# Performance work log

Hardware: AMD Instinct MI355X
Metric: run time of the kernel (lower is better)

Reference implementation:

```python
import jax, jax.numpy as jnp
import numpy as np

C = 1536
MA = 1536
NEG_SLOPE = 0.2


def setup_inputs() -> dict:
    key = jax.random.key(0)
    ks = jax.random.split(key, 11)
    s = 1.0 / np.sqrt(C)

    def u(k, shape):
        return jax.random.uniform(k, shape, jnp.float32, -s, s)

    return {
        "x": jax.random.normal(ks[0], (1, C), jnp.float32),
        "lw0": u(ks[1], (C, C)), "lb0": u(ks[2], (C,)),
        "lw1": u(ks[3], (C, C)), "lb1": u(ks[4], (C,)),
        "lw2": u(ks[5], (1, C)), "lb2": u(ks[6], (1,)),
        "W_ih": u(ks[7], (3, C, C)), "b_ih": u(ks[8], (3, C)),
        "W_hh": u(ks[9], (3, C, C)), "b_hh": u(ks[10], (3, C)),
        "max_atoms": MA,
    }


def reference(x, lw0, lb0, lw1, lb1, lw2, lb2, W_ih, b_ih, W_hh, b_hh, max_atoms):
    c_dim = x.shape[-1]
    x = x.reshape(1, c_dim)

    act = lambda v: jax.nn.leaky_relu(v, NEG_SLOPE)
    # LinearOutputStack(channels, 3, out_channels=1): 2 hidden layers + output head
    h = act(x @ lw0.T + lb0)
    h = act(h @ lw1.T + lb1)
    l = h @ lw2.T + lb2                       # [1, 1]
    length = jnp.clip(jnp.abs(l), 0.0, 0.9999)
    c = jnp.floor(length[0, 0] * max_atoms).astype(jnp.int32) + 1  # #valid steps

    hid0 = jnp.zeros((3, c_dim), x.dtype).at[0].set(x[0])  # hid[0] = x
    inp0 = jnp.zeros((c_dim,), x.dtype)

    def step(carry, _):
        inp, hid = carry
        cur = inp
        new_hid = []
        for layer in range(3):  # stacked relu-RNN, one timestep
            nh = jax.nn.relu(cur @ W_ih[layer].T + b_ih[layer]
                             + hid[layer] @ W_hh[layer].T + b_hh[layer])
            new_hid.append(nh)
            cur = nh
        return (cur, jnp.stack(new_hid)), cur

    _, seq = jax.lax.scan(step, (inp0, hid0), None, length=max_atoms)  # [MA, C]
    # Original returns only the first c rows; we pad with zeros for static shape.
    mask = (jnp.arange(max_atoms) < c)[:, None]
    seq = jnp.where(mask, seq, jnp.zeros((), seq.dtype))
    return seq, length
```

## Files before the change

kernel.cpp:

```cpp
#include <hip/hip_runtime.h>
#include <math.h>

#define C     1536
#define MA    1536
#define NWG   256
#define TPB   384
#define NEG   0.2f

#define WS_H0    0
#define WS_H1    (C)
#define WS_HB    (2*C)
#define WS_CNUM  (6*C)
#define WS_ARR   (6*C + 64)

#define WSCALE   (32760.0f * 39.191835884530846f)
#define WINV     (1.0f / WSCALE)

#define WL_WORDS (36 * 768)

__global__ void ve_init(unsigned* w) {
    for (int k = threadIdx.x; k < NWG * 16; k += blockDim.x)
        __hip_atomic_store(&w[WS_ARR + k], 0u, __ATOMIC_RELAXED, __HIP_MEMORY_SCOPE_AGENT);
}

__device__ __forceinline__ float wave_reduce(float v) {
#pragma unroll
    for (int off = 32; off > 0; off >>= 1) v += __shfl_xor(v, off, 64);
    return v;
}

__device__ __forceinline__ unsigned aloadu(const unsigned* p) {
    return __hip_atomic_load(p, __ATOMIC_RELAXED, __HIP_MEMORY_SCOPE_AGENT);
}

__device__ __forceinline__ float dot_row64(const float* __restrict__ W,
                                           const float* __restrict__ v, int lane) {
    const float4* W4 = (const float4*)W;
    const float4* v4 = (const float4*)v;
    float acc = 0.f;
#pragma unroll
    for (int j = 0; j < 6; ++j) {
        float4 a = W4[lane + 64 * j];
        float4 b = v4[lane + 64 * j];
        acc = fmaf(a.x, b.x, acc); acc = fmaf(a.y, b.y, acc);
        acc = fmaf(a.z, b.z, acc); acc = fmaf(a.w, b.w, acc);
    }
    return acc;
}

__device__ __forceinline__ float dot_w2(const int* __restrict__ wrow,
                                        const float2* __restrict__ hl, int lane) {
    float acc = 0.f;
#pragma unroll
    for (int mm = 0; mm < 12; ++mm) {
        int w   = wrow[mm * 64 + lane];
        float2 h = hl[mm * 64 + lane];
        acc = fmaf((float)(short)w, h.x, acc);
        acc = fmaf((float)(w >> 16), h.y, acc);
    }
    return acc;
}

__device__ __forceinline__ void stage_h(const float* __restrict__ hsrc,
                                        float2* __restrict__ hdst, int wave, int lane) {
    const unsigned long long* p = (const unsigned long long*)hsrc;
    const int i0 = wave * 128 + lane;
    const int i1 = i0 + 64;
    unsigned long long a = __hip_atomic_load(p + i0, __ATOMIC_RELAXED, __HIP_MEMORY_SCOPE_AGENT);
    unsigned long long b = __hip_atomic_load(p + i1, __ATOMIC_RELAXED, __HIP_MEMORY_SCOPE_AGENT);
    union { unsigned long long u; float2 f; } ua, ub;
    ua.u = a; ub.u = b;
    hdst[i0] = ua.f;
    hdst[i1] = ub.f;
}

__device__ __forceinline__ void bar_all(unsigned* arr, unsigned ep) {
    __syncthreads();
    if (threadIdx.x == 0) {
        __hip_atomic_store(arr + blockIdx.x * 16, ep, __ATOMIC_RELAXED, __HIP_MEMORY_SCOPE_AGENT);
        __builtin_amdgcn_fence(__ATOMIC_ACQUIRE, "agent");
    }
    if (threadIdx.x < 64) {
        const int i = threadIdx.x;
        unsigned m;
        do {
            unsigned f0 = aloadu(arr + (i      ) * 16);
            unsigned f1 = aloadu(arr + (i +  64) * 16);
            unsigned f2 = aloadu(arr + (i + 128) * 16);
            unsigned f3 = aloadu(arr + (i + 192) * 16);
            m = min(min(f0, f1), min(f2, f3));
            if (m < ep) __builtin_amdgcn_s_sleep(1);
        } while (m < ep);
    }
    __syncthreads();
}

extern __shared__ int wldsi[];

__global__ void __launch_bounds__(TPB, 1)
ve_main(const float* __restrict__ x,
        const float* __restrict__ lw0, const float* __restrict__ lb0,
        const float* __restrict__ lw1, const float* __restrict__ lb1,
        const float* __restrict__ lw2, const float* __restrict__ lb2,
        const float* __restrict__ Wih, const float* __restrict__ bih,
        const float* __restrict__ Whh, const float* __restrict__ bhh,
        float* __restrict__ out, float* __restrict__ wsf) {
    unsigned* wsu = (unsigned*)wsf;
    int*      wsi = (int*)wsf;
    unsigned* arr = wsu + WS_ARR;
    float*    hb  = wsf + WS_HB;
    float2*   hih = (float2*)(wldsi + WL_WORDS);
    float2*   hhh = hih + 768;
    const int tid  = threadIdx.x;
    const int b    = blockIdx.x;
    const int wave = tid >> 6;
    const int lane = tid & 63;
    const int row  = b * 6 + wave;

#pragma unroll
    for (int lm = 0; lm < 6; ++lm) {
        const int l = lm >> 1, m = lm & 1;
        const float* src = (m == 0 ? Wih : Whh) + ((size_t)l * C + row) * C;
        int* dst = wldsi + (lm * 6 + wave) * 768;
#pragma unroll
        for (int mm = 0; mm < 12; ++mm) {
            const int i = mm * 64 + lane;
            float2 wv = *(const float2*)(src + 2 * i);
            int q0 = (int)rintf(wv.x * WSCALE);
            int q1 = (int)rintf(wv.y * WSCALE);
            dst[i] = (q0 & 0xFFFF) | (q1 << 16);
        }
    }
    float bsum[3];
#pragma unroll
    for (int l = 0; l < 3; ++l) bsum[l] = bih[l * C + row] + bhh[l * C + row];

    {
        const int gtid = b * TPB + tid;
        if (gtid < 3 * C) {
            int slot = 1 + gtid / C;
            int idx  = gtid % C;
            float v  = (slot == 1) ? x[idx] : 0.f;
            __hip_atomic_store(&hb[slot * C + idx], v, __ATOMIC_RELAXED, __HIP_MEMORY_SCOPE_AGENT);
        }
    }

    {
        float acc = wave_reduce(dot_row64(lw0 + (size_t)row * C, x, lane));
        if (lane == 0) {
            float v = acc + lb0[row];
            v = (v > 0.f) ? v : NEG * v;
            __hip_atomic_store(&wsf[WS_H0 + row], v, __ATOMIC_RELAXED, __HIP_MEMORY_SCOPE_AGENT);
        }
    }
    bar_all(arr, 1);
    {
        float acc = wave_reduce(dot_row64(lw1 + (size_t)row * C, wsf + WS_H0, lane));
        if (lane == 0) {
            float v = acc + lb1[row];
            v = (v > 0.f) ? v : NEG * v;
            __hip_atomic_store(&wsf[WS_H1 + row], v, __ATOMIC_RELAXED, __HIP_MEMORY_SCOPE_AGENT);
        }
    }
    bar_all(arr, 2);
    if (row == 0) {
        float acc = wave_reduce(dot_row64(lw2, wsf + WS_H1, lane));
        if (lane == 0) {
            float l = acc + lb2[0];
            float length = fminf(fabsf(l), 0.9999f);
            __hip_atomic_store(&out[(size_t)MA * C], length, __ATOMIC_RELAXED,
                               __HIP_MEMORY_SCOPE_AGENT);
            __hip_atomic_store(&wsi[WS_CNUM], (int)floorf(length * (float)MA) + 1,
                               __ATOMIC_RELAXED, __HIP_MEMORY_SCOPE_AGENT);
        }
    }
    bar_all(arr, 3);
    const int csteps = wsi[WS_CNUM];

    stage_h(hb + 1 * C, hhh, wave, lane);
    float vout = 0.f;

    int k = 0;
    for (int t = 0; t < csteps; ++t) {
#pragma unroll
        for (int l = 0; l < 3; ++l, ++k) {
            if (tid < 64) {
                const unsigned* p = arr + tid * 16;
                const unsigned target = 3 + (unsigned)k;
                unsigned m;
                do {
                    unsigned f0 = aloadu(p);
                    unsigned f1 = aloadu(p +  64 * 16);
                    unsigned f2 = aloadu(p + 128 * 16);
                    unsigned f3 = aloadu(p + 192 * 16);
                    m = min(min(f0, f1), min(f2, f3));
                    if (m < target) __builtin_amdgcn_s_sleep(1);
                } while (m < target);
            }
            __syncthreads();
            stage_h(hb + ((k - 1) & 3) * C, hih, wave, lane);
            __syncthreads();
            {
                const int* wi = wldsi + ((l * 2 + 0) * 6 + wave) * 768;
                const int* wh = wldsi + ((l * 2 + 1) * 6 + wave) * 768;
                float acc = dot_w2(wi, hih, lane) + dot_w2(wh, hhh, lane);
                acc = wave_reduce(acc);
                if (lane == 0) {
                    float v = fmaxf(fmaf(acc, WINV, bsum[l]), 0.f);
                    __hip_atomic_store(&hb[(k & 3) * C + row], v, __ATOMIC_RELAXED,
                                       __HIP_MEMORY_SCOPE_AGENT);
                    vout = v;
                }
            }
            __syncthreads();
            if (tid == 0)
                __hip_atomic_store(arr + b * 16, 4 + (unsigned)k, __ATOMIC_RELAXED,
                                   __HIP_MEMORY_SCOPE_AGENT);
            if (l == 2 && lane == 0) out[(size_t)t * C + row] = vout;
            stage_h(hb + ((k + 2) & 3) * C, hhh, wave, lane);
        }
    }
}

extern "C" void kernel_launch(void* const* d_in, const int* in_sizes, int n_in,
                              void* d_out, int out_size, void* d_ws, size_t ws_size,
                              hipStream_t stream) {
    const float* x   = (const float*)d_in[0];
    const float* lw0 = (const float*)d_in[1];
    const float* lb0 = (const float*)d_in[2];
    const float* lw1 = (const float*)d_in[3];
    const float* lb1 = (const float*)d_in[4];
    const float* lw2 = (const float*)d_in[5];
    const float* lb2 = (const float*)d_in[6];
    const float* Wih = (const float*)d_in[7];
    const float* bih = (const float*)d_in[8];
    const float* Whh = (const float*)d_in[9];
    const float* bhh = (const float*)d_in[10];
    float* out = (float*)d_out;
    float* wsf = (float*)d_ws;

    const int lds_bytes = WL_WORDS * 4 + 2 * 768 * 8;
    hipFuncSetAttribute((const void*)ve_main,
                        hipFuncAttributeMaxDynamicSharedMemorySize, lds_bytes);

    hipMemsetAsync(d_out, 0, (size_t)out_size * sizeof(float), stream);
    hipLaunchKernelGGL(ve_init, dim3(1), dim3(256), 0, stream, (unsigned*)d_ws);

    void* args[] = {
        (void*)&x, (void*)&lw0, (void*)&lb0, (void*)&lw1, (void*)&lb1,
        (void*)&lw2, (void*)&lb2, (void*)&Wih, (void*)&bih, (void*)&Whh,
        (void*)&bhh, (void*)&out, (void*)&wsf
    };
    hipLaunchCooperativeKernel((const void*)ve_main, dim3(NWG), dim3(TPB),
                               args, lds_bytes, stream);
}
```

Baseline: 495.1 us.

## Replace grid barrier flags with epoch-tagged hidden-state words for dataflow sync

```diff
diff --git a/kernel.cpp b/kernel.cpp
--- a/kernel.cpp
+++ b/kernel.cpp
@@ -7,11 +7,13 @@
 #define TPB   384
 #define NEG   0.2f
 
+typedef unsigned long long u64;
+
 #define WS_H0    0
 #define WS_H1    (C)
-#define WS_HB    (2*C)
-#define WS_CNUM  (6*C)
-#define WS_ARR   (6*C + 64)
+#define WS_CNUM  (2*C)
+#define WS_ARR   (2*C + 64)
+#define WS_HT    8192
 
 #define WSCALE   (32760.0f * 39.191835884530846f)
 #define WINV     (1.0f / WSCALE)
@@ -28,8 +30,10 @@
     for (int off = 32; off > 0; off >>= 1) v += __shfl_xor(v, off, 64);
     return v;
 }
-
 __device__ __forceinline__ unsigned aloadu(const unsigned* p) {
+    return __hip_atomic_load(p, __ATOMIC_RELAXED, __HIP_MEMORY_SCOPE_AGENT);
+}
+__device__ __forceinline__ u64 aload64(const u64* p) {
     return __hip_atomic_load(p, __ATOMIC_RELAXED, __HIP_MEMORY_SCOPE_AGENT);
 }
 
@@ -48,30 +52,17 @@
     return acc;
 }
 
-__device__ __forceinline__ float dot_w2(const int* __restrict__ wrow,
-                                        const float2* __restrict__ hl, int lane) {
+__device__ __forceinline__ float dot_i16(const int* __restrict__ wrow,
+                                         const float* __restrict__ h, int lane) {
     float acc = 0.f;
 #pragma unroll
     for (int mm = 0; mm < 12; ++mm) {
-        int w   = wrow[mm * 64 + lane];
-        float2 h = hl[mm * 64 + lane];
-        acc = fmaf((float)(short)w, h.x, acc);
-        acc = fmaf((float)(w >> 16), h.y, acc);
+        int w = wrow[mm * 64 + lane];
+        float2 hv = *(const float2*)(h + 2 * (mm * 64 + lane));
+        acc = fmaf((float)(short)w, hv.x, acc);
+        acc = fmaf((float)(w >> 16), hv.y, acc);
     }
     return acc;
-}
-
-__device__ __forceinline__ void stage_h(const float* __restrict__ hsrc,
-                                        float2* __restrict__ hdst, int wave, int lane) {
-    const unsigned long long* p = (const unsigned long long*)hsrc;
-    const int i0 = wave * 128 + lane;
-    const int i1 = i0 + 64;
-    unsigned long long a = __hip_atomic_load(p + i0, __ATOMIC_RELAXED, __HIP_MEMORY_SCOPE_AGENT);
-    unsigned long long b = __hip_atomic_load(p + i1, __ATOMIC_RELAXED, __HIP_MEMORY_SCOPE_AGENT);
-    union { unsigned long long u; float2 f; } ua, ub;
-    ua.u = a; ub.u = b;
-    hdst[i0] = ua.f;
-    hdst[i1] = ub.f;
 }
 
 __device__ __forceinline__ void bar_all(unsigned* arr, unsigned ep) {
@@ -95,6 +86,36 @@
     __syncthreads();
 }
 
+__device__ __forceinline__ void stage_cell(const u64* __restrict__ ht, int k,
+                                           float* __restrict__ Lih, float* __restrict__ Lhh,
+                                           int wave, int lane) {
+    const int bi = wave * 256 + lane * 4;
+    const u64* shh = ht + ((k + 1) & 3) * 1536 + bi;
+    const u64* sih = ht + ((k - 1) & 3) * 1536 + bi;
+    const unsigned thh = (unsigned)(k + 13);
+    const unsigned tih = (unsigned)(k + 15);
+    u64 b0, b1, b2, b3;
+    for (;;) {
+        b0 = aload64(shh); b1 = aload64(shh + 1); b2 = aload64(shh + 2); b3 = aload64(shh + 3);
+        if ((unsigned)(b0 >> 32) == thh && (unsigned)(b1 >> 32) == thh &&
+            (unsigned)(b2 >> 32) == thh && (unsigned)(b3 >> 32) == thh) break;
+        __builtin_amdgcn_s_sleep(1);
+    }
+    float4 hv;
+    hv.x = __uint_as_float((unsigned)b0); hv.y = __uint_as_float((unsigned)b1);
+    hv.z = __uint_as_float((unsigned)b2); hv.w = __uint_as_float((unsigned)b3);
+    *(float4*)(Lhh + bi) = hv;
+    for (;;) {
+        b0 = aload64(sih); b1 = aload64(sih + 1); b2 = aload64(sih + 2); b3 = aload64(sih + 3);
+        if ((unsigned)(b0 >> 32) == tih && (unsigned)(b1 >> 32) == tih &&
+            (unsigned)(b2 >> 32) == tih && (unsigned)(b3 >> 32) == tih) break;
+        __builtin_amdgcn_s_sleep(1);
+    }
+    hv.x = __uint_as_float((unsigned)b0); hv.y = __uint_as_float((unsigned)b1);
+    hv.z = __uint_as_float((unsigned)b2); hv.w = __uint_as_float((unsigned)b3);
+    *(float4*)(Lih + bi) = hv;
+}
+
 extern __shared__ int wldsi[];
 
 __global__ void __launch_bounds__(TPB, 1)
@@ -108,9 +129,8 @@
     unsigned* wsu = (unsigned*)wsf;
     int*      wsi = (int*)wsf;
     unsigned* arr = wsu + WS_ARR;
-    float*    hb  = wsf + WS_HB;
-    float2*   hih = (float2*)(wldsi + WL_WORDS);
-    float2*   hhh = hih + 768;
+    u64*      ht  = (u64*)(wsf + WS_HT);
+    float*    Lb  = (float*)(wldsi + WL_WORDS);
     const int tid  = threadIdx.x;
     const int b    = blockIdx.x;
     const int wave = tid >> 6;
@@ -141,7 +161,9 @@
             int slot = 1 + gtid / C;
             int idx  = gtid % C;
             float v  = (slot == 1) ? x[idx] : 0.f;
-            __hip_atomic_store(&hb[slot * C + idx], v, __ATOMIC_RELAXED, __HIP_MEMORY_SCOPE_AGENT);
+            u64 w = ((u64)(unsigned)(slot + 12) << 32) | (u64)__float_as_uint(v);
+            __hip_atomic_store(&ht[slot * 1536 + idx], w, __ATOMIC_RELAXED,
+                               __HIP_MEMORY_SCOPE_AGENT);
         }
     }
 
@@ -177,47 +199,25 @@
     bar_all(arr, 3);
     const int csteps = wsi[WS_CNUM];
 
-    stage_h(hb + 1 * C, hhh, wave, lane);
-    float vout = 0.f;
-
     int k = 0;
     for (int t = 0; t < csteps; ++t) {
 #pragma unroll
         for (int l = 0; l < 3; ++l, ++k) {
-            if (tid < 64) {
-                const unsigned* p = arr + tid * 16;
-                const unsigned target = 3 + (unsigned)k;
-                unsigned m;
-                do {
-                    unsigned f0 = aloadu(p);
-                    unsigned f1 = aloadu(p +  64 * 16);
-                    unsigned f2 = aloadu(p + 128 * 16);
-                    unsigned f3 = aloadu(p + 192 * 16);
-                    m = min(min(f0, f1), min(f2, f3));
-                    if (m < target) __builtin_amdgcn_s_sleep(1);
-                } while (m < target);
+            float* Lih = Lb + (k & 1) * 1536;
+            float* Lhh = Lb + 3072 + (k & 1) * 1536;
+            stage_cell(ht, k, Lih, Lhh, wave, lane);
+            __syncthreads();
+            const int* wi = wldsi + ((l * 2 + 0) * 6 + wave) * 768;
+            const int* wh = wldsi + ((l * 2 + 1) * 6 + wave) * 768;
+            float acc = dot_i16(wi, Lih, lane) + dot_i16(wh, Lhh, lane);
+            acc = wave_reduce(acc);
+            if (lane == 0) {
+                float v = fmaxf(fmaf(acc, WINV, bsum[l]), 0.f);
+                u64 w = ((u64)(unsigned)(k + 16) << 32) | (u64)__float_as_uint(v);
+                __hip_atomic_store(&ht[(k & 3) * 1536 + row], w, __ATOMIC_RELAXED,
+                                   __HIP_MEMORY_SCOPE_AGENT);
+                if (l == 2) out[(size_t)t * C + row] = v;
             }
-            __syncthreads();
-            stage_h(hb + ((k - 1) & 3) * C, hih, wave, lane);
-            __syncthreads();
-            {
-                const int* wi = wldsi + ((l * 2 + 0) * 6 + wave) * 768;
-                const int* wh = wldsi + ((l * 2 + 1) * 6 + wave) * 768;
-                float acc = dot_w2(wi, hih, lane) + dot_w2(wh, hhh, lane);
-                acc = wave_reduce(acc);
-                if (lane == 0) {
-                    float v = fmaxf(fmaf(acc, WINV, bsum[l]), 0.f);
-                    __hip_atomic_store(&hb[(k & 3) * C + row], v, __ATOMIC_RELAXED,
-                                       __HIP_MEMORY_SCOPE_AGENT);
-                    vout = v;
-                }
-            }
-            __syncthreads();
-            if (tid == 0)
-                __hip_atomic_store(arr + b * 16, 4 + (unsigned)k, __ATOMIC_RELAXED,
-                                   __HIP_MEMORY_SCOPE_AGENT);
-            if (l == 2 && lane == 0) out[(size_t)t * C + row] = vout;
-            stage_h(hb + ((k + 2) & 3) * C, hhh, wave, lane);
         }
     }
 }
@@ -239,7 +239,7 @@
     float* out = (float*)d_out;
     float* wsf = (float*)d_ws;
 
-    const int lds_bytes = WL_WORDS * 4 + 2 * 768 * 8;
+    const int lds_bytes = WL_WORDS * 4 + 4 * 1536 * 4;
     hipFuncSetAttribute((const void*)ve_main,
                         hipFuncAttributeMaxDynamicSharedMemorySize, lds_bytes);
 
```

Result: slower. 719.9 us (+45.4%).

## Overlap hidden-state matvec with grid barrier wait using double-buffered LDS

Applied to the files above, without the earlier changes.

```diff
diff --git a/kernel.cpp b/kernel.cpp
--- a/kernel.cpp
+++ b/kernel.cpp
@@ -7,6 +7,8 @@
 #define TPB   384
 #define NEG   0.2f
 
+typedef unsigned long long u64;
+
 #define WS_H0    0
 #define WS_H1    (C)
 #define WS_HB    (2*C)
@@ -28,8 +30,10 @@
     for (int off = 32; off > 0; off >>= 1) v += __shfl_xor(v, off, 64);
     return v;
 }
-
 __device__ __forceinline__ unsigned aloadu(const unsigned* p) {
+    return __hip_atomic_load(p, __ATOMIC_RELAXED, __HIP_MEMORY_SCOPE_AGENT);
+}
+__device__ __forceinline__ u64 aload64(const u64* p) {
     return __hip_atomic_load(p, __ATOMIC_RELAXED, __HIP_MEMORY_SCOPE_AGENT);
 }
 
@@ -48,30 +52,30 @@
     return acc;
 }
 
-__device__ __forceinline__ float dot_w2(const int* __restrict__ wrow,
-                                        const float2* __restrict__ hl, int lane) {
+__device__ __forceinline__ float dot_i16(const int* __restrict__ wrow,
+                                         const float* __restrict__ h, int lane) {
     float acc = 0.f;
 #pragma unroll
     for (int mm = 0; mm < 12; ++mm) {
-        int w   = wrow[mm * 64 + lane];
-        float2 h = hl[mm * 64 + lane];
-        acc = fmaf((float)(short)w, h.x, acc);
-        acc = fmaf((float)(w >> 16), h.y, acc);
+        int w = wrow[mm * 64 + lane];
+        float2 hv = *(const float2*)(h + 2 * (mm * 64 + lane));
+        acc = fmaf((float)(short)w, hv.x, acc);
+        acc = fmaf((float)(w >> 16), hv.y, acc);
     }
     return acc;
 }
 
 __device__ __forceinline__ void stage_h(const float* __restrict__ hsrc,
-                                        float2* __restrict__ hdst, int wave, int lane) {
-    const unsigned long long* p = (const unsigned long long*)hsrc;
+                                        float* __restrict__ hdst, int wave, int lane) {
+    const u64* p = (const u64*)hsrc;
     const int i0 = wave * 128 + lane;
     const int i1 = i0 + 64;
-    unsigned long long a = __hip_atomic_load(p + i0, __ATOMIC_RELAXED, __HIP_MEMORY_SCOPE_AGENT);
-    unsigned long long b = __hip_atomic_load(p + i1, __ATOMIC_RELAXED, __HIP_MEMORY_SCOPE_AGENT);
-    union { unsigned long long u; float2 f; } ua, ub;
+    u64 a = aload64(p + i0);
+    u64 b = aload64(p + i1);
+    union { u64 u; float2 f; } ua, ub;
     ua.u = a; ub.u = b;
-    hdst[i0] = ua.f;
-    hdst[i1] = ub.f;
+    ((float2*)hdst)[i0] = ua.f;
+    ((float2*)hdst)[i1] = ub.f;
 }
 
 __device__ __forceinline__ void bar_all(unsigned* arr, unsigned ep) {
@@ -109,8 +113,8 @@
     int*      wsi = (int*)wsf;
     unsigned* arr = wsu + WS_ARR;
     float*    hb  = wsf + WS_HB;
-    float2*   hih = (float2*)(wldsi + WL_WORDS);
-    float2*   hhh = hih + 768;
+    float*    Lih = (float*)(wldsi + WL_WORDS);
+    float*    Lhh = Lih + 1536;
     const int tid  = threadIdx.x;
     const int b    = blockIdx.x;
     const int wave = tid >> 6;
@@ -177,13 +181,15 @@
     bar_all(arr, 3);
     const int csteps = wsi[WS_CNUM];
 
-    stage_h(hb + 1 * C, hhh, wave, lane);
-    float vout = 0.f;
+    stage_h(hb + 1 * C, Lhh, wave, lane);
+    __syncthreads();
 
     int k = 0;
     for (int t = 0; t < csteps; ++t) {
 #pragma unroll
         for (int l = 0; l < 3; ++l, ++k) {
+            const int* wh = wldsi + ((l * 2 + 1) * 6 + wave) * 768;
+            float hh_acc = dot_i16(wh, Lhh + (k & 1) * 1536, lane);
             if (tid < 64) {
                 const unsigned* p = arr + tid * 16;
                 const unsigned target = 3 + (unsigned)k;
@@ -198,26 +204,24 @@
                 } while (m < target);
             }
             __syncthreads();
-            stage_h(hb + ((k - 1) & 3) * C, hih, wave, lane);
+            stage_h(hb + ((k - 1) & 3) * C, Lih, wave, lane);
+            stage_h(hb + ((k + 2) & 3) * C, Lhh + ((k + 1) & 1) * 1536, wave, lane);
             __syncthreads();
+            float vout;
             {
                 const int* wi = wldsi + ((l * 2 + 0) * 6 + wave) * 768;
-                const int* wh = wldsi + ((l * 2 + 1) * 6 + wave) * 768;
-                float acc = dot_w2(wi, hih, lane) + dot_w2(wh, hhh, lane);
+                float acc = hh_acc + dot_i16(wi, Lih, lane);
                 acc = wave_reduce(acc);
-                if (lane == 0) {
-                    float v = fmaxf(fmaf(acc, WINV, bsum[l]), 0.f);
-                    __hip_atomic_store(&hb[(k & 3) * C + row], v, __ATOMIC_RELAXED,
+                vout = fmaxf(fmaf(acc, WINV, bsum[l]), 0.f);
+                if (lane == 0)
+                    __hip_atomic_store(&hb[(k & 3) * C + row], vout, __ATOMIC_RELAXED,
                                        __HIP_MEMORY_SCOPE_AGENT);
-                    vout = v;
-                }
             }
             __syncthreads();
             if (tid == 0)
                 __hip_atomic_store(arr + b * 16, 4 + (unsigned)k, __ATOMIC_RELAXED,
                                    __HIP_MEMORY_SCOPE_AGENT);
             if (l == 2 && lane == 0) out[(size_t)t * C + row] = vout;
-            stage_h(hb + ((k + 2) & 3) * C, hhh, wave, lane);
         }
     }
 }
@@ -239,7 +243,7 @@
     float* out = (float*)d_out;
     float* wsf = (float*)d_ws;
 
-    const int lds_bytes = WL_WORDS * 4 + 2 * 768 * 8;
+    const int lds_bytes = WL_WORDS * 4 + 3 * 1536 * 4;
     hipFuncSetAttribute((const void*)ve_main,
                         hipFuncAttributeMaxDynamicSharedMemorySize, lds_bytes);
 
```

New measurement: 444.4 us. 1.11x faster.
